# Optimization experiments

Hardware: AMD Instinct MI355X
Metric: run time of the kernel (lower is better)

Reference implementation:

```python
import jax, jax.numpy as jnp
import numpy as np


def setup_inputs() -> dict:
    key = jax.random.key(0)
    ks = jax.random.split(key, 12)
    B, S, D, Q = 16, 2048, 1024, 64
    std = 1.0 / np.sqrt(D)
    return {
        "raw": jax.random.normal(ks[0], (B, S, D), jnp.float32),
        "post_dec": jax.random.normal(ks[1], (B, S, D), jnp.float32),
        "mask": jnp.ones((B, S), dtype=bool),
        "questions": jax.random.uniform(ks[2], (Q, D), jnp.float32),
        "Wk": jax.random.normal(ks[3], (D, D), jnp.float32) * std,
        "bk": jnp.zeros((D,), jnp.float32),
        "Wi": jax.random.normal(ks[4], (1, D), jnp.float32) * std,
        "bi": jnp.zeros((1,), jnp.float32),
        "Wo": jax.random.normal(ks[5], (D, D), jnp.float32) * std,
        "bo": jnp.zeros((D,), jnp.float32),
        "Wu1": jax.random.normal(ks[6], (1, D), jnp.float32) * std,
        "bu1": jnp.zeros((1,), jnp.float32),
        "Wu2": jax.random.normal(ks[7], (1, D), jnp.float32) * std,
        "bu2": jnp.zeros((1,), jnp.float32),
        "b1": jax.random.uniform(ks[8], (1,), jnp.float32),
    }


def reference(raw, post_dec, mask, questions, Wk, bk, Wi, bi, Wo, bo, Wu1, bu1, Wu2, bu2, b1):
    D = raw.shape[-1]
    Q = questions.shape[0]
    inv_sqrt_d = jnp.float32(1.0 / np.sqrt(D))
    inv_sqrt_q = jnp.float32(1.0 / np.sqrt(Q))

    # ---- create_A_matrix: write external memory A [Q, D] ----
    k = raw @ Wk.T + bk                                   # [B,S,D]
    v = raw * jax.nn.sigmoid(raw @ Wi.T + bi)             # ignore gate, [B,S,D]
    scores = jnp.einsum('qd,bsd->bqs', questions, k) * inv_sqrt_d  # [B,Q,S]
    scores = jnp.where(mask[:, None, :], scores, jnp.float32(-1e9))
    attn = jax.nn.softmax(scores, axis=-1)
    A = jnp.einsum('bqs,bsd->qd', attn, v) / jnp.float32(raw.shape[0])  # mean over batch

    # ---- get_data_from_A_matrix: read memory ----
    ko = post_dec @ Wo.T + bo                              # [B,S,D]
    s2 = jnp.einsum('bsd,qd->bsq', ko, questions) * inv_sqrt_q  # [B,S,Q]
    A2 = jax.nn.softmax(s2, axis=-1) @ A                   # [B,S,D]
    gate = jax.nn.sigmoid((post_dec @ Wu1.T + bu1) + (A2 @ Wu2.T + bu2) + b1)  # [B,S,1]
    return post_dec + A2 * gate
```

## Files before the change

### kernel.cpp

```cpp
#include <hip/hip_runtime.h>
#include <math.h>

#define NBATCH 16
#define SEQ    2048
#define BS     32768
#define DIM    1024
#define NQ     64
#define CKS    68
#define INV_SQRT_D 0.03125f
#define INV_SQRT_Q 0.125f

#define OFF_QT   0
#define OFF_CKT  65536
#define OFF_COT  135168
#define OFF_S1   204800
#define OFF_G2   2334720
#define OFF_A    2367488
#define OFF_BO   2433024
#define OFF_AW   2433088
#define OFF_CKP  2433152
#define OFF_COP  2474112
#define OFF_W2B  2515072
#define OFF_AMT  3563648

typedef short bf16x8 __attribute__((ext_vector_type(8)));
typedef float f32x4 __attribute__((ext_vector_type(4)));

union V8 { uint4 u4; bf16x8 s8; uint32_t u[4]; };

__device__ __forceinline__ f32x4 mfma16(bf16x8 a, bf16x8 b, f32x4 c) {
  return __builtin_amdgcn_mfma_f32_16x16x32_bf16(a, b, c, 0, 0, 0);
}
__device__ __forceinline__ uint32_t f2b(float f) { return __float_as_uint(f); }
__device__ __forceinline__ uint32_t packtr(float lo, float hi) {
  return __builtin_amdgcn_perm(f2b(hi), f2b(lo), 0x07060302u);
}
__device__ __forceinline__ uint32_t rne1(float f) {
  uint32_t u = f2b(f);
  return (u + 0x7FFFu + ((u >> 16) & 1u)) >> 16;
}
__device__ __forceinline__ uint32_t packrne(float lo, float hi) {
  return rne1(lo) | (rne1(hi) << 16);
}
__device__ __forceinline__ bf16x8 ldg8(const unsigned short* p) {
  V8 v; v.u4 = *(const uint4*)p; return v.s8;
}
__device__ __forceinline__ bf16x8 pack8(const float* p) {
  float4 a = *(const float4*)p;
  float4 b = *(const float4*)(p + 4);
  V8 v;
  v.u[0] = packtr(a.x, a.y);
  v.u[1] = packtr(a.z, a.w);
  v.u[2] = packtr(b.x, b.y);
  v.u[3] = packtr(b.z, b.w);
  return v.s8;
}

__global__ __launch_bounds__(256) void kpre(const float* __restrict__ questions,
                                            const float* __restrict__ bo,
                                            const float* __restrict__ Wi,
                                            const float* __restrict__ Wu1,
                                            float* __restrict__ ws) {
  __shared__ float red[4];
  float* qT    = ws + OFF_QT;
  float* CKT   = ws + OFF_CKT;
  float* COT   = ws + OFF_COT;
  float* biasO = ws + OFF_BO;
  int bid = blockIdx.x, tid = threadIdx.x;
  if (bid < 64) {
    int q = bid;
    float acc = 0.f;
    for (int e = tid; e < DIM; e += 256) {
      float v = questions[q*DIM + e];
      qT[e*NQ + q] = v;
      acc += v * bo[e];
    }
    for (int off = 32; off > 0; off >>= 1) acc += __shfl_xor(acc, off, 64);
    if ((tid & 63) == 0) red[tid >> 6] = acc;
    __syncthreads();
    if (tid == 0) biasO[q] = red[0] + red[1] + red[2] + red[3];
  } else {
    int r = bid - 64;
    int h = r & 1;
    const float* src = (r < 2) ? Wi : Wu1;
    float* dst = (r < 2) ? CKT : COT;
    int d = h*512 + tid;
    dst[d*CKS + 64] = src[d];
    d += 256;
    dst[d*CKS + 64] = src[d];
  }
}

__global__ __launch_bounds__(256) void k0_proj(const float* __restrict__ Wk,
                                               const float* __restrict__ Wo,
                                               float* __restrict__ ws) {
  const float* qT = ws + OFF_QT;
  int bid = blockIdx.x;
  int mat = bid & 1;
  int kc  = (bid >> 1) & 3;
  int dt  = bid >> 3;
  const float* W = mat ? Wo : Wk;
  float* dest = ws + (mat ? OFF_COT : OFF_CKT);
  int d0 = dt * 64, e0 = kc * 256;
  __shared__ __align__(16) float aL[32*CKS];
  __shared__ __align__(16) float bL[32*CKS];
  int tid = threadIdx.x;
  int tx = tid & 15, ty = tid >> 4;
  float acc[4][4] = {};
  for (int ek = e0; ek < e0 + 256; ek += 32) {
    for (int idx = tid; idx < 32*64; idx += 256) {
      int kk = idx >> 6, j = idx & 63;
      aL[kk*CKS + j] = qT[(ek + kk)*NQ + j];
      bL[kk*CKS + j] = W[(size_t)(ek + kk)*DIM + d0 + j];
    }
    __syncthreads();
#pragma unroll
    for (int kk = 0; kk < 32; kk++) {
      float4 av = *(const float4*)&aL[kk*CKS + ty*4];
      float4 bv = *(const float4*)&bL[kk*CKS + tx*4];
      float a[4] = {av.x, av.y, av.z, av.w};
      float b[4] = {bv.x, bv.y, bv.z, bv.w};
#pragma unroll
      for (int r = 0; r < 4; ++r)
#pragma unroll
        for (int c = 0; c < 4; ++c)
          acc[r][c] += a[r] * b[c];
    }
    __syncthreads();
  }
#pragma unroll
  for (int r = 0; r < 4; ++r)
#pragma unroll
    for (int c = 0; c < 4; ++c)
      atomicAdd(&dest[(d0 + tx*4 + c)*CKS + ty*4 + r], acc[r][c]);
}

__global__ __launch_bounds__(256) void kpack(float* __restrict__ ws) {
  int bid = blockIdx.x;
  int row = bid % 80;
  int mat = bid / 80;
  const float* src = ws + (mat ? OFF_COT : OFF_CKT);
  unsigned short* dst = (unsigned short*)(ws + (mat ? OFF_COP : OFF_CKP));
  int d = threadIdx.x * 4;
  float v[4];
#pragma unroll
  for (int i = 0; i < 4; ++i)
    v[i] = (row <= 64) ? src[(d + i)*CKS + row] : 0.f;
  uint2 o;
  o.x = packrne(v[0], v[1]);
  o.y = packrne(v[2], v[3]);
  *(uint2*)(dst + (size_t)row*DIM + d) = o;
}

__global__ __launch_bounds__(256) void k1_scores(const float* __restrict__ raw,
                                                 float* __restrict__ ws) {
  const unsigned short* CKp = (const unsigned short*)(ws + OFF_CKP);
  float* S1 = ws + OFF_S1;
  int tid = threadIdx.x;
  int wave = tid >> 6, lane = tid & 63, lm = lane & 15, quad = lane >> 4;
  int tb = blockIdx.x*128 + wave*32;
  f32x4 acc[5][2] = {};
  for (int k0 = 0; k0 < DIM; k0 += 32) {
    bf16x8 af[5];
#pragma unroll
    for (int mt = 0; mt < 5; ++mt)
      af[mt] = ldg8(CKp + (size_t)(mt*16 + lm)*DIM + k0 + quad*8);
    bf16x8 bfr[2];
#pragma unroll
    for (int nt = 0; nt < 2; ++nt)
      bfr[nt] = pack8(raw + (size_t)(tb + nt*16 + lm)*DIM + k0 + quad*8);
#pragma unroll
    for (int mt = 0; mt < 5; ++mt)
#pragma unroll
      for (int nt = 0; nt < 2; ++nt)
        acc[mt][nt] = mfma16(af[mt], bfr[nt], acc[mt][nt]);
  }
#pragma unroll
  for (int mt = 0; mt < 4; ++mt)
#pragma unroll
    for (int nt = 0; nt < 2; ++nt)
#pragma unroll
      for (int reg = 0; reg < 4; ++reg)
        S1[(size_t)(mt*16 + quad*4 + reg)*BS + tb + nt*16 + lm] = acc[mt][nt][reg];
  if (quad == 0) {
#pragma unroll
    for (int nt = 0; nt < 2; ++nt)
      S1[(size_t)64*BS + tb + nt*16 + lm] = acc[4][nt][0];
  }
}

__global__ __launch_bounds__(256) void k2g(const float* __restrict__ biP,
                                           float* __restrict__ ws) {
  const float* S1 = ws + OFF_S1;
  float* g2 = ws + OFF_G2;
  int t = blockIdx.x*256 + threadIdx.x;
  float v = S1[(size_t)64*BS + t] + biP[0];
  g2[t] = (1.f / (1.f + __expf(-v))) * (1.f / (float)NBATCH);
}

__global__ __launch_bounds__(256) void k2_softmax(float* __restrict__ ws) {
  const float* S1 = ws + OFF_S1;
  const float* g2 = ws + OFF_G2;
  uint32_t* w2u = (uint32_t*)(ws + OFF_W2B);
  __shared__ float redA[4];
  __shared__ float redB[4];
  int bid = blockIdx.x;
  int q = bid & 63, b = bid >> 6;
  int tid = threadIdx.x, wave = tid >> 6, lane = tid & 63;
  const float* row = S1 + (size_t)q*BS + b*SEQ + tid*8;
  float4 xa = *(const float4*)row;
  float4 xb = *(const float4*)(row + 4);
  float x[8] = {xa.x, xa.y, xa.z, xa.w, xb.x, xb.y, xb.z, xb.w};
#pragma unroll
  for (int i = 0; i < 8; ++i) x[i] *= INV_SQRT_D;
  float m = -1e30f;
#pragma unroll
  for (int i = 0; i < 8; ++i) m = fmaxf(m, x[i]);
  for (int off = 32; off > 0; off >>= 1) m = fmaxf(m, __shfl_xor(m, off, 64));
  if (lane == 0) redA[wave] = m;
  __syncthreads();
  m = fmaxf(fmaxf(redA[0], redA[1]), fmaxf(redA[2], redA[3]));
  float e[8];
  float s = 0.f;
#pragma unroll
  for (int i = 0; i < 8; ++i) { e[i] = __expf(x[i] - m); s += e[i]; }
  for (int off = 32; off > 0; off >>= 1) s += __shfl_xor(s, off, 64);
  if (lane == 0) redB[wave] = s;
  __syncthreads();
  s = redB[0] + redB[1] + redB[2] + redB[3];
  float inv = 1.f / s;
  const float* g2b = g2 + b*SEQ + tid*8;
  float4 ga = *(const float4*)g2b;
  float4 gb = *(const float4*)(g2b + 4);
  float g[8] = {ga.x, ga.y, ga.z, ga.w, gb.x, gb.y, gb.z, gb.w};
  float w[8];
#pragma unroll
  for (int i = 0; i < 8; ++i) w[i] = e[i] * inv * g[i];
  uint4 o;
  o.x = packtr(w[0], w[1]);
  o.y = packtr(w[2], w[3]);
  o.z = packtr(w[4], w[5]);
  o.w = packtr(w[6], w[7]);
  *(uint4*)&w2u[((size_t)q*BS + b*SEQ + tid*8) >> 1] = o;
}

#define K3STR 36
__global__ __launch_bounds__(256) void k3_accA(const float* __restrict__ raw,
                                               float* __restrict__ ws) {
  const unsigned short* w2b = (const unsigned short*)(ws + OFF_W2B);
  float* A = ws + OFF_A;
  int bid = blockIdx.x;
  int dt = bid & 7, tc = bid >> 3;
  int d0 = dt*128;
  int tid = threadIdx.x;
  int wave = tid >> 6, lane = tid & 63, lm = lane & 15, quad = lane >> 4;
  int pq = tid & 7;
  int dr = tid >> 3;
  __shared__ __align__(16) uint32_t ldsB[128*K3STR];
  f32x4 acc[4][2] = {};
  for (int tk = tc*1024; tk < tc*1024 + 1024; tk += 64) {
    float4 rv[8];
#pragma unroll
    for (int r = 0; r < 8; ++r)
      rv[r] = *(const float4*)&raw[(size_t)(tk + pq*8 + r)*DIM + d0 + dr*4];
    __syncthreads();
    int pc = ((pq ^ (dr & 7)) << 2);
#pragma unroll
    for (int j = 0; j < 4; ++j) {
      const float* f0 = (const float*)&rv[0];
      uint4 wv;
      wv.x = packtr(((const float*)&rv[0])[j], ((const float*)&rv[1])[j]);
      wv.y = packtr(((const float*)&rv[2])[j], ((const float*)&rv[3])[j]);
      wv.z = packtr(((const float*)&rv[4])[j], ((const float*)&rv[5])[j]);
      wv.w = packtr(((const float*)&rv[6])[j], ((const float*)&rv[7])[j]);
      (void)f0;
      *(uint4*)&ldsB[(dr*4 + j)*K3STR + pc] = wv;
    }
    __syncthreads();
#pragma unroll
    for (int ks = 0; ks < 2; ++ks) {
      bf16x8 af[4];
#pragma unroll
      for (int mt = 0; mt < 4; ++mt)
        af[mt] = ldg8(w2b + (size_t)(mt*16 + lm)*BS + tk + ks*32 + quad*8);
      bf16x8 bfr[2];
#pragma unroll
      for (int nt = 0; nt < 2; ++nt) {
        int rowd = wave*32 + nt*16 + lm;
        int pcr = (((ks*4 + quad) ^ ((rowd >> 2) & 7)) << 2);
        V8 v; v.u4 = *(const uint4*)&ldsB[rowd*K3STR + pcr];
        bfr[nt] = v.s8;
      }
#pragma unroll
      for (int mt = 0; mt < 4; ++mt)
#pragma unroll
        for (int nt = 0; nt < 2; ++nt)
          acc[mt][nt] = mfma16(af[mt], bfr[nt], acc[mt][nt]);
    }
  }
#pragma unroll
  for (int mt = 0; mt < 4; ++mt)
#pragma unroll
    for (int nt = 0; nt < 2; ++nt)
#pragma unroll
      for (int reg = 0; reg < 4; ++reg)
        atomicAdd(&A[(mt*16 + quad*4 + reg)*DIM + d0 + wave*32 + nt*16 + lm],
                  acc[mt][nt][reg]);
}

__global__ __launch_bounds__(256) void k3b_aw(const float* __restrict__ Wu2,
                                              float* __restrict__ ws) {
  const float* A = ws + OFF_A;
  float* aw = ws + OFF_AW;
  unsigned short* at = (unsigned short*)(ws + OFF_AMT);
  __shared__ float red[4];
  int q = blockIdx.x, tid = threadIdx.x;
  float acc = 0.f;
  for (int d = tid; d < DIM; d += 256) {
    float v = A[q*DIM + d];
    acc += v * Wu2[d];
    at[(size_t)d*NQ + q] = (unsigned short)rne1(v);
  }
  for (int off = 32; off > 0; off >>= 1) acc += __shfl_xor(acc, off, 64);
  if ((tid & 63) == 0) red[tid >> 6] = acc;
  __syncthreads();
  if (tid == 0) aw[q] = red[0] + red[1] + red[2] + red[3];
}

#define T4STR 85
#define WSTR  72
__global__ __launch_bounds__(256) void k4_phase2(const float* __restrict__ post_dec,
                                                 const float* __restrict__ bu1p,
                                                 const float* __restrict__ bu2p,
                                                 const float* __restrict__ b1p,
                                                 float* __restrict__ out,
                                                 float* __restrict__ ws) {
  const unsigned short* COp = (const unsigned short*)(ws + OFF_COP);
  const unsigned short* AmT = (const unsigned short*)(ws + OFF_AMT);
  const float* biasO = ws + OFF_BO;
  const float* aw    = ws + OFF_AW;
  __shared__ __align__(16) float T[64*T4STR];
  __shared__ __align__(16) unsigned short wL[64*WSTR];
  __shared__ float gateL[64], bOL[64], awL[64];
  int t0 = blockIdx.x * 64;
  int tid = threadIdx.x;
  int wave = tid >> 6, lane = tid & 63, lm = lane & 15, quad = lane >> 4;
  if (tid < 64) { bOL[tid] = biasO[tid]; awL[tid] = aw[tid]; }

  f32x4 acc[5] = {};
  for (int k0 = 0; k0 < DIM; k0 += 32) {
    bf16x8 af = pack8(post_dec + (size_t)(t0 + wave*16 + lm)*DIM + k0 + quad*8);
#pragma unroll
    for (int nt = 0; nt < 5; ++nt) {
      bf16x8 b = ldg8(COp + (size_t)(nt*16 + lm)*DIM + k0 + quad*8);
      acc[nt] = mfma16(af, b, acc[nt]);
    }
  }
#pragma unroll
  for (int nt = 0; nt < 5; ++nt)
#pragma unroll
    for (int reg = 0; reg < 4; ++reg)
      T[(wave*16 + quad*4 + reg)*T4STR + nt*16 + lm] = acc[nt][reg];
  __syncthreads();

  if (tid < 64) {
    float* Tr = T + tid*T4STR;
    float m = -1e30f;
#pragma unroll 8
    for (int j = 0; j < 64; ++j) {
      float y = (Tr[j] + bOL[j]) * INV_SQRT_Q;
      Tr[j] = y;
      m = fmaxf(m, y);
    }
    float s = 0.f;
#pragma unroll 8
    for (int j = 0; j < 64; ++j) {
      float e = __expf(Tr[j] - m);
      Tr[j] = e;
      s += e;
    }
    float inv = 1.f / s;
    float u2 = 0.f;
    uint32_t* wr = (uint32_t*)(wL + tid*WSTR);
#pragma unroll 8
    for (int j2 = 0; j2 < 32; ++j2) {
      float w0 = Tr[2*j2] * inv;
      float w1 = Tr[2*j2 + 1] * inv;
      u2 += w0 * awL[2*j2] + w1 * awL[2*j2 + 1];
      wr[j2] = packtr(w0, w1);
    }
    float garg = Tr[64] + bu1p[0] + u2 + bu2p[0] + b1p[0];
    gateL[tid] = 1.f / (1.f + __expf(-garg));
  }
  __syncthreads();

  float gv[4][4];
#pragma unroll
  for (int mt = 0; mt < 4; ++mt)
#pragma unroll
    for (int reg = 0; reg < 4; ++reg)
      gv[mt][reg] = gateL[mt*16 + quad*4 + reg];
  for (int d0 = 0; d0 < DIM; d0 += 256) {
    f32x4 acc2[4][4] = {};
#pragma unroll
    for (int ks = 0; ks < 2; ++ks) {
      bf16x8 am[4];
#pragma unroll
      for (int mt = 0; mt < 4; ++mt) {
        V8 v; v.u4 = *(const uint4*)&wL[(mt*16 + lm)*WSTR + ks*32 + quad*8];
        am[mt] = v.s8;
      }
      bf16x8 bn[4];
#pragma unroll
      for (int nt = 0; nt < 4; ++nt)
        bn[nt] = ldg8(AmT + (size_t)(d0 + wave*64 + nt*16 + lm)*NQ + ks*32 + quad*8);
#pragma unroll
      for (int mt = 0; mt < 4; ++mt)
#pragma unroll
        for (int nt = 0; nt < 4; ++nt)
          acc2[mt][nt] = mfma16(am[mt], bn[nt], acc2[mt][nt]);
    }
#pragma unroll
    for (int mt = 0; mt < 4; ++mt)
#pragma unroll
      for (int nt = 0; nt < 4; ++nt)
#pragma unroll
        for (int reg = 0; reg < 4; ++reg) {
          int t = t0 + mt*16 + quad*4 + reg;
          int d = d0 + wave*64 + nt*16 + lm;
          out[(size_t)t*DIM + d] = post_dec[(size_t)t*DIM + d]
                                 + acc2[mt][nt][reg] * gv[mt][reg];
        }
  }
}

extern "C" void kernel_launch(void* const* d_in, const int* in_sizes, int n_in,
                              void* d_out, int out_size, void* d_ws, size_t ws_size,
                              hipStream_t stream) {
  const float* raw       = (const float*)d_in[0];
  const float* post_dec  = (const float*)d_in[1];
  const float* questions = (const float*)d_in[3];
  const float* Wk        = (const float*)d_in[4];
  const float* Wi        = (const float*)d_in[6];
  const float* bi        = (const float*)d_in[7];
  const float* Wo        = (const float*)d_in[8];
  const float* bo        = (const float*)d_in[9];
  const float* Wu1       = (const float*)d_in[10];
  const float* bu1       = (const float*)d_in[11];
  const float* Wu2       = (const float*)d_in[12];
  const float* bu2       = (const float*)d_in[13];
  const float* b1        = (const float*)d_in[14];
  float* out = (float*)d_out;
  float* ws  = (float*)d_ws;

  hipMemsetAsync(ws + OFF_CKT, 0, (size_t)2*DIM*CKS*sizeof(float), stream);
  hipMemsetAsync(ws + OFF_A,   0, (size_t)NQ*DIM*sizeof(float), stream);

  kpre<<<68, 256, 0, stream>>>(questions, bo, Wi, Wu1, ws);
  k0_proj<<<128, 256, 0, stream>>>(Wk, Wo, ws);
  kpack<<<160, 256, 0, stream>>>(ws);
  k1_scores<<<256, 256, 0, stream>>>(raw, ws);
  k2g<<<128, 256, 0, stream>>>(bi, ws);
  k2_softmax<<<1024, 256, 0, stream>>>(ws);
  k3_accA<<<256, 256, 0, stream>>>(raw, ws);
  k3b_aw<<<64, 256, 0, stream>>>(Wu2, ws);
  k4_phase2<<<512, 256, 0, stream>>>(post_dec, bu1, bu2, b1, out, ws);
}
```

Before: 549.9 us.

## Split K across blocks and waves to raise parallelism in score, accumulate and phase-2 kernels

k1_scores now splits the D reduction into two halves across blocks and combines them with atomicAdd into a zeroed S1, launching four times as many blocks. k3_accA halves the token chunk per block to double the grid. k4_phase2 processes 32 tokens per block with waves split across K halves, and parallelizes the row softmax and gate over 8 lanes per row using shuffles. The aim is better CU occupancy and latency hiding on a 256-CU GPU, at the cost of atomic traffic, an extra memset of S1 and more redundant weight loads per token.

```diff
diff --git a/kernel.cpp b/kernel.cpp
--- a/kernel.cpp
+++ b/kernel.cpp
@@ -158,35 +158,26 @@
   float* S1 = ws + OFF_S1;
   int tid = threadIdx.x;
   int wave = tid >> 6, lane = tid & 63, lm = lane & 15, quad = lane >> 4;
-  int tb = blockIdx.x*128 + wave*32;
-  f32x4 acc[5][2] = {};
-  for (int k0 = 0; k0 < DIM; k0 += 32) {
-    bf16x8 af[5];
-#pragma unroll
-    for (int mt = 0; mt < 5; ++mt)
-      af[mt] = ldg8(CKp + (size_t)(mt*16 + lm)*DIM + k0 + quad*8);
-    bf16x8 bfr[2];
-#pragma unroll
-    for (int nt = 0; nt < 2; ++nt)
-      bfr[nt] = pack8(raw + (size_t)(tb + nt*16 + lm)*DIM + k0 + quad*8);
-#pragma unroll
-    for (int mt = 0; mt < 5; ++mt)
-#pragma unroll
-      for (int nt = 0; nt < 2; ++nt)
-        acc[mt][nt] = mfma16(af[mt], bfr[nt], acc[mt][nt]);
+  int bid = blockIdx.x;
+  int kh = bid & 1;
+  int tb = (bid >> 1) * 64 + wave * 16;
+  f32x4 acc[5] = {};
+  int k0beg = kh * 512;
+  for (int k0 = k0beg; k0 < k0beg + 512; k0 += 32) {
+    bf16x8 bfr = pack8(raw + (size_t)(tb + lm)*DIM + k0 + quad*8);
+#pragma unroll
+    for (int mt = 0; mt < 5; ++mt) {
+      bf16x8 af = ldg8(CKp + (size_t)(mt*16 + lm)*DIM + k0 + quad*8);
+      acc[mt] = mfma16(af, bfr, acc[mt]);
+    }
   }
 #pragma unroll
   for (int mt = 0; mt < 4; ++mt)
 #pragma unroll
-    for (int nt = 0; nt < 2; ++nt)
-#pragma unroll
-      for (int reg = 0; reg < 4; ++reg)
-        S1[(size_t)(mt*16 + quad*4 + reg)*BS + tb + nt*16 + lm] = acc[mt][nt][reg];
-  if (quad == 0) {
-#pragma unroll
-    for (int nt = 0; nt < 2; ++nt)
-      S1[(size_t)64*BS + tb + nt*16 + lm] = acc[4][nt][0];
-  }
+    for (int reg = 0; reg < 4; ++reg)
+      atomicAdd(&S1[(size_t)(mt*16 + quad*4 + reg)*BS + tb + lm], acc[mt][reg]);
+  if (quad == 0)
+    atomicAdd(&S1[(size_t)64*BS + tb + lm], acc[4][0]);
 }
 
 __global__ __launch_bounds__(256) void k2g(const float* __restrict__ biP,
@@ -258,7 +249,7 @@
   int dr = tid >> 3;
   __shared__ __align__(16) uint32_t ldsB[128*K3STR];
   f32x4 acc[4][2] = {};
-  for (int tk = tc*1024; tk < tc*1024 + 1024; tk += 64) {
+  for (int tk = tc*512; tk < tc*512 + 512; tk += 64) {
     float4 rv[8];
 #pragma unroll
     for (int r = 0; r < 8; ++r)
@@ -329,6 +320,7 @@
 
 #define T4STR 85
 #define WSTR  72
+#define BM4   32
 __global__ __launch_bounds__(256) void k4_phase2(const float* __restrict__ post_dec,
                                                  const float* __restrict__ bu1p,
                                                  const float* __restrict__ bu2p,
@@ -339,17 +331,19 @@
   const unsigned short* AmT = (const unsigned short*)(ws + OFF_AMT);
   const float* biasO = ws + OFF_BO;
   const float* aw    = ws + OFF_AW;
-  __shared__ __align__(16) float T[64*T4STR];
-  __shared__ __align__(16) unsigned short wL[64*WSTR];
-  __shared__ float gateL[64], bOL[64], awL[64];
-  int t0 = blockIdx.x * 64;
+  __shared__ __align__(16) float T[2][BM4][T4STR];
+  __shared__ __align__(16) unsigned short wL[BM4*WSTR];
+  __shared__ float gateL[BM4], bOL[64], awL[64];
+  int t0 = blockIdx.x * BM4;
   int tid = threadIdx.x;
   int wave = tid >> 6, lane = tid & 63, lm = lane & 15, quad = lane >> 4;
   if (tid < 64) { bOL[tid] = biasO[tid]; awL[tid] = aw[tid]; }
 
+  int mh = wave & 1;
+  int kh = wave >> 1;
   f32x4 acc[5] = {};
-  for (int k0 = 0; k0 < DIM; k0 += 32) {
-    bf16x8 af = pack8(post_dec + (size_t)(t0 + wave*16 + lm)*DIM + k0 + quad*8);
+  for (int k0 = kh*512; k0 < kh*512 + 512; k0 += 32) {
+    bf16x8 af = pack8(post_dec + (size_t)(t0 + mh*16 + lm)*DIM + k0 + quad*8);
 #pragma unroll
     for (int nt = 0; nt < 5; ++nt) {
       bf16x8 b = ldg8(COp + (size_t)(nt*16 + lm)*DIM + k0 + quad*8);
@@ -360,53 +354,61 @@
   for (int nt = 0; nt < 5; ++nt)
 #pragma unroll
     for (int reg = 0; reg < 4; ++reg)
-      T[(wave*16 + quad*4 + reg)*T4STR + nt*16 + lm] = acc[nt][reg];
+      T[kh][mh*16 + quad*4 + reg][nt*16 + lm] = acc[nt][reg];
   __syncthreads();
 
-  if (tid < 64) {
-    float* Tr = T + tid*T4STR;
-    float m = -1e30f;
-#pragma unroll 8
-    for (int j = 0; j < 64; ++j) {
-      float y = (Tr[j] + bOL[j]) * INV_SQRT_Q;
-      Tr[j] = y;
-      m = fmaxf(m, y);
-    }
-    float s = 0.f;
-#pragma unroll 8
-    for (int j = 0; j < 64; ++j) {
-      float e = __expf(Tr[j] - m);
-      Tr[j] = e;
-      s += e;
+  {
+    int row = tid >> 3, sub = tid & 7;
+    const float* T0 = T[0][row];
+    const float* T1 = T[1][row];
+    float x[8];
+#pragma unroll
+    for (int i = 0; i < 8; ++i) {
+      int j = sub*8 + i;
+      x[i] = (T0[j] + T1[j] + bOL[j]) * INV_SQRT_Q;
+    }
+    float m = x[0];
+#pragma unroll
+    for (int i = 1; i < 8; ++i) m = fmaxf(m, x[i]);
+    for (int off = 1; off < 8; off <<= 1) m = fmaxf(m, __shfl_xor(m, off, 64));
+    float e[8], s = 0.f, sa = 0.f;
+#pragma unroll
+    for (int i = 0; i < 8; ++i) {
+      e[i] = __expf(x[i] - m);
+      s += e[i];
+      sa += e[i] * awL[sub*8 + i];
+    }
+    for (int off = 1; off < 8; off <<= 1) {
+      s  += __shfl_xor(s, off, 64);
+      sa += __shfl_xor(sa, off, 64);
     }
     float inv = 1.f / s;
-    float u2 = 0.f;
-    uint32_t* wr = (uint32_t*)(wL + tid*WSTR);
-#pragma unroll 8
-    for (int j2 = 0; j2 < 32; ++j2) {
-      float w0 = Tr[2*j2] * inv;
-      float w1 = Tr[2*j2 + 1] * inv;
-      u2 += w0 * awL[2*j2] + w1 * awL[2*j2 + 1];
-      wr[j2] = packtr(w0, w1);
-    }
-    float garg = Tr[64] + bu1p[0] + u2 + bu2p[0] + b1p[0];
-    gateL[tid] = 1.f / (1.f + __expf(-garg));
+    uint32_t* wr = (uint32_t*)(wL + row*WSTR);
+#pragma unroll
+    for (int i2 = 0; i2 < 4; ++i2)
+      wr[sub*4 + i2] = packtr(e[2*i2]*inv, e[2*i2+1]*inv);
+    if (sub == 0) {
+      float u1 = T0[64] + T1[64];
+      float u2 = sa * inv;
+      float garg = u1 + bu1p[0] + u2 + bu2p[0] + b1p[0];
+      gateL[row] = 1.f / (1.f + __expf(-garg));
+    }
   }
   __syncthreads();
 
-  float gv[4][4];
-#pragma unroll
-  for (int mt = 0; mt < 4; ++mt)
+  float gv[2][4];
+#pragma unroll
+  for (int mt = 0; mt < 2; ++mt)
 #pragma unroll
     for (int reg = 0; reg < 4; ++reg)
       gv[mt][reg] = gateL[mt*16 + quad*4 + reg];
   for (int d0 = 0; d0 < DIM; d0 += 256) {
-    f32x4 acc2[4][4] = {};
+    f32x4 acc2[2][4] = {};
 #pragma unroll
     for (int ks = 0; ks < 2; ++ks) {
-      bf16x8 am[4];
-#pragma unroll
-      for (int mt = 0; mt < 4; ++mt) {
+      bf16x8 am[2];
+#pragma unroll
+      for (int mt = 0; mt < 2; ++mt) {
         V8 v; v.u4 = *(const uint4*)&wL[(mt*16 + lm)*WSTR + ks*32 + quad*8];
         am[mt] = v.s8;
       }
@@ -415,13 +417,13 @@
       for (int nt = 0; nt < 4; ++nt)
         bn[nt] = ldg8(AmT + (size_t)(d0 + wave*64 + nt*16 + lm)*NQ + ks*32 + quad*8);
 #pragma unroll
-      for (int mt = 0; mt < 4; ++mt)
+      for (int mt = 0; mt < 2; ++mt)
 #pragma unroll
         for (int nt = 0; nt < 4; ++nt)
           acc2[mt][nt] = mfma16(am[mt], bn[nt], acc2[mt][nt]);
     }
 #pragma unroll
-    for (int mt = 0; mt < 4; ++mt)
+    for (int mt = 0; mt < 2; ++mt)
 #pragma unroll
       for (int nt = 0; nt < 4; ++nt)
 #pragma unroll
@@ -454,15 +456,16 @@
   float* ws  = (float*)d_ws;
 
   hipMemsetAsync(ws + OFF_CKT, 0, (size_t)2*DIM*CKS*sizeof(float), stream);
+  hipMemsetAsync(ws + OFF_S1,  0, (size_t)65*BS*sizeof(float), stream);
   hipMemsetAsync(ws + OFF_A,   0, (size_t)NQ*DIM*sizeof(float), stream);
 
   kpre<<<68, 256, 0, stream>>>(questions, bo, Wi, Wu1, ws);
   k0_proj<<<128, 256, 0, stream>>>(Wk, Wo, ws);
   kpack<<<160, 256, 0, stream>>>(ws);
-  k1_scores<<<256, 256, 0, stream>>>(raw, ws);
+  k1_scores<<<1024, 256, 0, stream>>>(raw, ws);
   k2g<<<128, 256, 0, stream>>>(bi, ws);
   k2_softmax<<<1024, 256, 0, stream>>>(ws);
-  k3_accA<<<256, 256, 0, stream>>>(raw, ws);
+  k3_accA<<<512, 256, 0, stream>>>(raw, ws);
   k3b_aw<<<64, 256, 0, stream>>>(Wu2, ws);
-  k4_phase2<<<512, 256, 0, stream>>>(post_dec, bu1, bu2, b1, out, ws);
-}
+  k4_phase2<<<1024, 256, 0, stream>>>(post_dec, bu1, bu2, b1, out, ws);
+}
```

After: 597.8 us. 1.09x slower.
